# Kernel optimization log

Hardware: AMD Instinct MI355X
Metric: run time of the kernel (lower is better)

## Reference

```python
import jax, jax.numpy as jnp
import numpy as np
import math

B, S, HID = 2, 4096, 768
H, D, M = 12, 64, 64  # heads, head_dim, num_landmarks
CK = 33  # conv kernel size


def setup_inputs() -> dict:
    key = jax.random.key(0)
    ks = jax.random.split(key, 4)
    x = jax.random.normal(ks[0], (B, S, HID), dtype=jnp.float32)
    qkv_w = jax.random.normal(ks[1], (3 * HID, HID), dtype=jnp.float32) * 0.02
    qkv_b = jnp.zeros((3 * HID,), dtype=jnp.float32)
    conv_w = jax.random.normal(ks[2], (H, 1, CK, 1), dtype=jnp.float32) * 0.02
    out_w = jax.random.normal(ks[3], (HID, HID), dtype=jnp.float32) * 0.02
    out_b = jnp.zeros((HID,), dtype=jnp.float32)
    return {"x": x, "qkv_w": qkv_w, "qkv_b": qkv_b, "conv_w": conv_w,
            "out_w": out_w, "out_b": out_b}


def iterative_inv(mat, n_iter=6):
    # Newton-Schulz pseudo-inverse on [B,H,M,M]
    I = jnp.eye(mat.shape[-1], dtype=mat.dtype)
    K = mat
    a = jnp.abs(K)
    scale = 1.0 / (jnp.max(jnp.sum(a, axis=-2)) * jnp.max(jnp.sum(a, axis=-1)))
    V = scale * jnp.swapaxes(K, -1, -2)
    for _ in range(n_iter):
        KV = K @ V
        V = 0.25 * V @ (13.0 * I - KV @ (15.0 * I - KV @ (7.0 * I - KV)))
    return V


def reference(x, qkv_w, qkv_b, conv_w, out_w, out_b):
    scale = 1.0 / math.sqrt(D)
    qkv = x @ qkv_w.T + qkv_b  # [B,S,3*HID]
    q, k, v = jnp.split(qkv, 3, axis=-1)
    # [B,H,S,D]
    Q = q.reshape(B, S, H, D).transpose(0, 2, 1, 3)
    K = k.reshape(B, S, H, D).transpose(0, 2, 1, 3)
    V = v.reshape(B, S, H, D).transpose(0, 2, 1, 3)
    # landmark means over contiguous segments of size S//M
    seg = S // M
    Q_l = Q.reshape(B, H, M, seg, D).mean(axis=-2)  # [B,H,M,D]
    K_l = K.reshape(B, H, M, seg, D).mean(axis=-2)
    kernel_1 = jax.nn.softmax(jnp.einsum('bhsd,bhmd->bhsm', Q, K_l) * scale, axis=-1)
    kernel_2 = jax.nn.softmax(jnp.einsum('bhmd,bhnd->bhmn', Q_l, K_l) * scale, axis=-1)
    kernel_3 = jax.nn.softmax(jnp.einsum('bhmd,bhsd->bhms', Q_l, K) * scale, axis=-1)
    X = kernel_1 @ (iterative_inv(kernel_2) @ (kernel_3 @ V))  # [B,H,S,D]
    # depthwise conv over sequence dim: NCHW with C=H, spatial=(S,D), kernel (CK,1)
    pad = CK // 2
    conv_out = jax.lax.conv_general_dilated(
        V, conv_w, window_strides=(1, 1), padding=((pad, pad), (0, 0)),
        dimension_numbers=('NCHW', 'OIHW', 'NCHW'), feature_group_count=H)
    X = X + conv_out
    X = X.transpose(0, 2, 1, 3).reshape(B, S, HID)
    X = X @ out_w.T + out_b
    return X
```

## Files before the change

kernel.cpp:

```cpp
#include <hip/hip_runtime.h>
#include <math.h>

#define B_   2
#define S_   4096
#define HID_ 768
#define H_   12
#define D_   64
#define M_   64
#define CK_  33
#define BH_  (B_*H_)
#define KD_  768
#define NCH_ 32
#define SC_  128

typedef float  f32x4  __attribute__((ext_vector_type(4)));
typedef _Float16 f16x8 __attribute__((ext_vector_type(8)));
typedef unsigned short u16;

__device__ __forceinline__ u16 f2h_bits(float f) {
  union { _Float16 h; u16 u; } c; c.h = (_Float16)f; return c.u;
}
__device__ __forceinline__ float h2f(u16 b) {
  union { _Float16 h; u16 u; } c; c.u = b; return (float)c.h;
}
__device__ __forceinline__ void cvt8_hl(const float4 a, const float4 b,
                                        f16x8* hi, f16x8* lo) {
  const float v[8] = {a.x, a.y, a.z, a.w, b.x, b.y, b.z, b.w};
  f16x8 H, L;
#pragma unroll
  for (int e = 0; e < 8; ++e) {
    const _Float16 hh = (_Float16)v[e];
    H[e] = hh;
    L[e] = (_Float16)(v[e] - (float)hh);
  }
  *hi = H; *lo = L;
}

__device__ __forceinline__ void gld16(const void* g, void* l) {
  __builtin_amdgcn_global_load_lds(
      (const __attribute__((address_space(1))) void*)g,
      (__attribute__((address_space(3))) void*)l, 16, 0, 0);
}

#define N8X  786432
#define N8WQ 221184
#define N8WO 73728
__global__ __launch_bounds__(256) void split3(
    const float* __restrict__ x, const float* __restrict__ qkv_w,
    const float* __restrict__ out_w,
    u16* __restrict__ Xh, u16* __restrict__ Wqh, u16* __restrict__ Woh)
{
  const int i = blockIdx.x * 256 + threadIdx.x;
  const float* src; u16* dst; int j;
  if (i < N8X)                 { src = x;     dst = Xh;  j = i; }
  else if (i < N8X + N8WQ)     { src = qkv_w; dst = Wqh; j = i - N8X; }
  else if (i < N8X + N8WQ + N8WO) { src = out_w; dst = Woh; j = i - N8X - N8WQ; }
  else return;
  const float4 a = ((const float4*)src)[2 * j], b = ((const float4*)src)[2 * j + 1];
  const float v[8] = {a.x, a.y, a.z, a.w, b.x, b.y, b.z, b.w};
  union { u16 u[8]; uint4 q; } hv;
#pragma unroll
  for (int e = 0; e < 8; ++e) hv.u[e] = f2h_bits(v[e]);
  ((uint4*)dst)[j] = hv.q;
}

template<int MODE, int PROD>
__global__ __launch_bounds__(256) void gemm_mfma(
    const u16* __restrict__ Ahg, const u16* __restrict__ Alg,
    const u16* __restrict__ Bhg,
    const float* __restrict__ bias,
    float* __restrict__ oF, u16* __restrict__ oQ, u16* __restrict__ oK,
    u16* __restrict__ oV,
    float* __restrict__ Ql, float* __restrict__ Kl, u16* __restrict__ Klh)
{
  constexpr int BM = (MODE == 0) ? 128 : 64;
  constexpr int BN = (MODE == 0) ? 64 : 128;
  constexpr int NBX = (MODE == 0) ? 36 : 6;
  constexpr int WM = BM / 2, WN = BN / 2;
  constexpr int MF = WM / 16, NF = WN / 16;
  constexpr int AINST = BM / 64, BINST = BN / 64;
  constexpr int ABUF = BM * 32;
  constexpr int BUFSZ = ABUF * PROD + BN * 32;
  constexpr int NT = KD_ / 32;
  constexpr int NWG = NBX * (8192 / BM);
  constexpr int CPX = NWG / 8;
  constexpr int NLOADS = AINST * PROD + BINST;

  __shared__ __align__(16) u16 lds[2][BUFSZ];

  const int tid = threadIdx.x;
  const int lin = blockIdx.y * NBX + blockIdx.x;
  const int swb = (lin & 7) * CPX + (lin >> 3);
  const int m0 = (swb / NBX) * BM;
  const int n0 = (swb % NBX) * BN;

  const int wave = tid >> 6, lane = tid & 63;
  const int wm = wave >> 1, wn = wave & 1;
  const int lr = lane & 15, kg = lane >> 4;

  const int srow = tid >> 2;
  const int swz_s = (tid >> 3) & 3;
  const int sk = ((tid & 3) ^ swz_s) * 8;

  const u16* pAh = Ahg + (size_t)(m0 + srow) * KD_ + sk;
  const u16* pAl = (PROD == 2) ? (Alg + (size_t)(m0 + srow) * KD_ + sk) : nullptr;
  const u16* pBh = Bhg + (size_t)(n0 + srow) * KD_ + sk;

  f32x4 acc[MF][NF];
#pragma unroll
  for (int i = 0; i < MF; ++i)
#pragma unroll
    for (int j = 0; j < NF; ++j) acc[i][j] = (f32x4){0.f, 0.f, 0.f, 0.f};

  const int rsw = (lr >> 1) & 3;
  const int kq = (kg ^ rsw) * 8;
  const int abase = (wm * WM + lr) * 32 + kq;
  const int bbase = (wn * WN + lr) * 32 + kq;

#define STAGE_(buf, kt) do {                                              \
    const size_t go_ = (size_t)(kt) * 32;                                 \
    u16* L_ = &lds[buf][0];                                               \
    gld16(pAh + go_, L_ + tid * 8);                                       \
    if (AINST == 2) gld16(pAh + go_ + 64 * KD_, L_ + 2048 + tid * 8);     \
    if (PROD == 2) {                                                      \
      gld16(pAl + go_, L_ + ABUF + tid * 8);                              \
      if (AINST == 2) gld16(pAl + go_ + 64 * KD_, L_ + ABUF + 2048 + tid * 8); \
    }                                                                     \
    gld16(pBh + go_, L_ + ABUF * PROD + tid * 8);                         \
    if (BINST == 2) gld16(pBh + go_ + 64 * KD_, L_ + ABUF * PROD + 2048 + tid * 8); \
  } while (0)

  STAGE_(0, 0);

  int cur = 0;
  for (int kt = 0; kt < NT; ++kt) {
    if (kt + 1 < NT) {
      STAGE_(cur ^ 1, kt + 1);
      if constexpr (NLOADS == 3)
        asm volatile("s_waitcnt vmcnt(3)" ::: "memory");
      else
        asm volatile("s_waitcnt vmcnt(4)" ::: "memory");
    } else {
      asm volatile("s_waitcnt vmcnt(0)" ::: "memory");
    }
    __builtin_amdgcn_s_barrier();
    __builtin_amdgcn_sched_barrier(0);

    const u16* L_ = &lds[cur][0];
    f16x8 ah[MF], al[MF], bh[NF];
#pragma unroll
    for (int i = 0; i < MF; ++i) {
      ah[i] = *(const f16x8*)&L_[abase + i * 512];
      if (PROD == 2) al[i] = *(const f16x8*)&L_[ABUF + abase + i * 512];
    }
#pragma unroll
    for (int j = 0; j < NF; ++j)
      bh[j] = *(const f16x8*)&L_[ABUF * PROD + bbase + j * 512];
#pragma unroll
    for (int i = 0; i < MF; ++i)
#pragma unroll
      for (int j = 0; j < NF; ++j) {
        acc[i][j] = __builtin_amdgcn_mfma_f32_16x16x32_f16(ah[i], bh[j], acc[i][j], 0, 0, 0);
        if (PROD == 2)
          acc[i][j] = __builtin_amdgcn_mfma_f32_16x16x32_f16(al[i], bh[j], acc[i][j], 0, 0, 0);
      }

    __builtin_amdgcn_sched_barrier(0);
    __builtin_amdgcn_s_barrier();
    cur ^= 1;
  }
#undef STAGE_

  if (MODE == 0) {
    const int part = n0 / 768;
    const int h0 = (n0 - part * 768) >> 6;
    u16* base = (part == 0) ? oQ : ((part == 1) ? oK : oV);
#pragma unroll
    for (int i = 0; i < MF; ++i) {
      const int mbase = m0 + wm * WM + i * 16 + kg * 4;
#pragma unroll
      for (int j = 0; j < NF; ++j) {
        const int d = wn * WN + j * 16 + lr;
        const float bv = bias[n0 + d];
#pragma unroll
        for (int r = 0; r < 4; ++r) {
          const int row = mbase + r;
          const int b = row >> 12, s = row & (S_ - 1);
          base[(((size_t)(b * H_ + h0) * S_ + s) << 6) + d] = f2h_bits(acc[i][j][r] + bv);
        }
      }
    }
    if (part < 2) {
      const int rowseg = m0 + wm * WM;
      const int b = rowseg >> 12;
      const int seg = (rowseg & (S_ - 1)) >> 6;
      const int bhh = b * H_ + h0;
      float* dst = (part == 0) ? Ql : Kl;
#pragma unroll
      for (int j = 0; j < NF; ++j) {
        float sj = 0.f;
#pragma unroll
        for (int i = 0; i < MF; ++i)
#pragma unroll
          for (int r = 0; r < 4; ++r) sj += acc[i][j][r];
        sj += __shfl_xor(sj, 16);
        sj += __shfl_xor(sj, 32);
        if (kg == 0) {
          const int d = wn * WN + j * 16 + lr;
          const float lm = sj * (1.f / 64.f) + bias[n0 + d];
          dst[((size_t)bhh * M_ + seg) * 64 + d] = lm;
          if (part == 1) Klh[((size_t)bhh * M_ + seg) * 64 + d] = f2h_bits(lm);
        }
      }
    }
  } else {
#pragma unroll
    for (int i = 0; i < MF; ++i) {
      const int mbase = m0 + wm * WM + i * 16 + kg * 4;
#pragma unroll
      for (int j = 0; j < NF; ++j) {
        const int ncol = n0 + wn * WN + j * 16 + lr;
        const float bv = bias[ncol];
#pragma unroll
        for (int r = 0; r < 4; ++r) {
          const int row = mbase + r;
          oF[(size_t)row * HID_ + ncol] = acc[i][j][r] + bv;
        }
      }
    }
  }
}

__global__ __launch_bounds__(256) void kernel2_softmax(
    const float* __restrict__ Ql, const float* __restrict__ Kl,
    float* __restrict__ K2, float* __restrict__ colmax, float* __restrict__ rowmax)
{
  __shared__ float Qs[64][68], Ks[64][68], S2[64][68];
  __shared__ float red1[64], red2[64];
  const int bh = blockIdx.x, tid = threadIdx.x;
  for (int idx = tid; idx < 4096; idx += 256) {
    const int r = idx >> 6, c = idx & 63;
    Qs[r][c] = Ql[(size_t)bh * 4096 + idx];
    Ks[r][c] = Kl[(size_t)bh * 4096 + idx];
  }
  __syncthreads();
  for (int idx = tid; idx < 4096; idx += 256) {
    const int r = idx >> 6, c = idx & 63;
    float dot = 0.f;
#pragma unroll
    for (int k = 0; k < 64; k += 4) {
      const float4 a = *(const float4*)&Qs[r][k];
      const float4 b = *(const float4*)&Ks[c][k];
      dot += a.x * b.x + a.y * b.y + a.z * b.z + a.w * b.w;
    }
    S2[r][c] = dot * 0.125f;
  }
  __syncthreads();
  if (tid < 64) {
    const int r = tid;
    float mx = -1e30f;
    for (int c = 0; c < 64; ++c) mx = fmaxf(mx, S2[r][c]);
    float sum = 0.f;
    for (int c = 0; c < 64; ++c) { const float e = expf(S2[r][c] - mx); S2[r][c] = e; sum += e; }
    const float inv = 1.f / sum;
    for (int c = 0; c < 64; ++c) S2[r][c] *= inv;
  }
  __syncthreads();
  for (int idx = tid; idx < 4096; idx += 256)
    K2[(size_t)bh * 4096 + idx] = S2[idx >> 6][idx & 63];
  if (tid < 64) {
    float cs = 0.f, rs = 0.f;
    for (int m = 0; m < 64; ++m) { cs += S2[m][tid]; rs += S2[tid][m]; }
    red1[tid] = cs; red2[tid] = rs;
  }
  __syncthreads();
  if (tid == 0) {
    float mc = 0.f, mr = 0.f;
    for (int i = 0; i < 64; ++i) { mc = fmaxf(mc, red1[i]); mr = fmaxf(mr, red2[i]); }
    colmax[bh] = mc; rowmax[bh] = mr;
  }
}

__device__ inline void mm64w(float (*C)[68], float (*A)[68], float (*B)[68], int tid)
{
  const int r0 = (tid >> 4) * 2;
  const int c0 = (tid & 15) * 4;
  float acc[2][4];
#pragma unroll
  for (int i = 0; i < 2; ++i)
#pragma unroll
    for (int j = 0; j < 4; ++j) acc[i][j] = 0.f;
  for (int k = 0; k < 64; k += 4) {
    float4 a[2], b[4];
#pragma unroll
    for (int i = 0; i < 2; ++i) a[i] = *(const float4*)&A[r0 + i][k];
#pragma unroll
    for (int j = 0; j < 4; ++j) b[j] = *(const float4*)&B[k + j][c0];
    const float bb[4][4] = {{b[0].x, b[0].y, b[0].z, b[0].w},
                            {b[1].x, b[1].y, b[1].z, b[1].w},
                            {b[2].x, b[2].y, b[2].z, b[2].w},
                            {b[3].x, b[3].y, b[3].z, b[3].w}};
    const float aa[2][4] = {{a[0].x, a[0].y, a[0].z, a[0].w},
                            {a[1].x, a[1].y, a[1].z, a[1].w}};
#pragma unroll
    for (int i = 0; i < 2; ++i)
#pragma unroll
      for (int j = 0; j < 4; ++j)
#pragma unroll
        for (int kk = 0; kk < 4; ++kk) acc[i][j] += aa[i][kk] * bb[kk][j];
  }
#pragma unroll
  for (int i = 0; i < 2; ++i)
    *(float4*)&C[r0 + i][c0] = make_float4(acc[i][0], acc[i][1], acc[i][2], acc[i][3]);
}

__global__ __launch_bounds__(512) void newton_combine(
    const float* __restrict__ K2, const float* __restrict__ colmax,
    const float* __restrict__ rowmax,
    const float* __restrict__ Opart, const float* __restrict__ mpart,
    const float* __restrict__ lpart, float* __restrict__ W2)
{
  __shared__ float A_[64][68], V_[64][68], KV_[64][68], T_[64][68], U_[64][68];
  __shared__ float scale_s;
  const int bh = blockIdx.x, tid = threadIdx.x;
  if (tid == 0) {
    float mc = 0.f, mr = 0.f;
    for (int i = 0; i < BH_; ++i) { mc = fmaxf(mc, colmax[i]); mr = fmaxf(mr, rowmax[i]); }
    scale_s = 1.f / (mc * mr);
  }
  for (int idx = tid; idx < 4096; idx += 512)
    A_[idx >> 6][idx & 63] = K2[(size_t)bh * 4096 + idx];
  __syncthreads();
  const float scale = scale_s;
  for (int idx = tid; idx < 4096; idx += 512) {
    const int r = idx >> 6, c = idx & 63;
    V_[r][c] = scale * A_[c][r];
  }
  __syncthreads();
  for (int it = 0; it < 6; ++it) {
    mm64w(KV_, A_, V_, tid); __syncthreads();
    for (int idx = tid; idx < 4096; idx += 512) {
      const int r = idx >> 6, c = idx & 63;
      T_[r][c] = (r == c ? 7.f : 0.f) - KV_[r][c];
    }
    __syncthreads();
    mm64w(U_, KV_, T_, tid); __syncthreads();
    for (int idx = tid; idx < 4096; idx += 512) {
      const int r = idx >> 6, c = idx & 63;
      T_[r][c] = (r == c ? 15.f : 0.f) - U_[r][c];
    }
    __syncthreads();
    mm64w(U_, KV_, T_, tid); __syncthreads();
    for (int idx = tid; idx < 4096; idx += 512) {
      const int r = idx >> 6, c = idx & 63;
      T_[r][c] = (r == c ? 13.f : 0.f) - U_[r][c];
    }
    __syncthreads();
    mm64w(U_, V_, T_, tid); __syncthreads();
    for (int idx = tid; idx < 4096; idx += 512) {
      const int r = idx >> 6, c = idx & 63;
      V_[r][c] = 0.25f * U_[r][c];
    }
    __syncthreads();
  }
  float (*W1s)[68] = A_;
  float (*C_)[68]  = KV_;
  float (*w_)[68]  = T_;
  if (tid < 64) {
    const int m = tid;
    float M = -1e30f;
    for (int j = 0; j < NCH_; ++j)
      M = fmaxf(M, mpart[((size_t)bh * NCH_ + j) * 64 + m]);
    float denom = 0.f;
    for (int j = 0; j < NCH_; ++j)
      denom += expf(mpart[((size_t)bh * NCH_ + j) * 64 + m] - M) *
               lpart[((size_t)bh * NCH_ + j) * 64 + m];
    const float inv = 1.f / denom;
    for (int j = 0; j < NCH_; ++j)
      w_[m][j] = expf(mpart[((size_t)bh * NCH_ + j) * 64 + m] - M) * inv;
  }
  __syncthreads();
  const int mgB = tid >> 4, dq = (tid & 15) * 4;
#pragma unroll
  for (int i = 0; i < 2; ++i) {
    const int m = mgB + 32 * i;
    float4 acc = make_float4(0.f, 0.f, 0.f, 0.f);
    for (int j = 0; j < NCH_; ++j) {
      const float ww = w_[m][j];
      const float4 o = *(const float4*)&Opart[(((size_t)bh * NCH_ + j) * 64 + m) * 64 + dq];
      acc.x += ww * o.x; acc.y += ww * o.y; acc.z += ww * o.z; acc.w += ww * o.w;
    }
    *(float4*)&W1s[m][dq] = acc;
  }
  __syncthreads();
  mm64w(C_, V_, W1s, tid);
  __syncthreads();
  for (int idx = tid; idx < 4096; idx += 512)
    W2[(size_t)bh * 4096 + idx] = C_[idx >> 6][idx & 63];
}

__global__ __launch_bounds__(256) void k3v_pass1(
    const float* __restrict__ Ql, const u16* __restrict__ Kh,
    const u16* __restrict__ Vh, float* __restrict__ Opart,
    float* __restrict__ mpart, float* __restrict__ lpart)
{
  __shared__ float P[64][129];
  __shared__ float red1[64][4], red2[64][4];

  const int ch = blockIdx.x;
  const int bh = blockIdx.y;
  const int tid = threadIdx.x;
  const int wave = tid >> 6, lane = tid & 63;
  const int lr = lane & 15, kg = lane >> 4;

  const float* Qlb = Ql + (size_t)bh * 4096;
  const u16*   Kb  = Kh + (size_t)bh * S_ * 64;
  const u16*   Vb  = Vh + (size_t)bh * S_ * 64;

  f16x8 ah[4][2], al[4][2];
#pragma unroll
  for (int mt = 0; mt < 4; ++mt)
#pragma unroll
    for (int kk = 0; kk < 2; ++kk) {
      const float* qr = Qlb + (size_t)(mt * 16 + lr) * 64 + kk * 32 + kg * 8;
      cvt8_hl(*(const float4*)qr, *(const float4*)(qr + 4), &ah[mt][kk], &al[mt][kk]);
    }

#pragma unroll
  for (int t = 0; t < 2; ++t) {
    const int s0 = (wave * 2 + t) * 16;
    const int srow = ch * SC_ + s0 + lr;
    f32x4 acc[4];
#pragma unroll
    for (int mt = 0; mt < 4; ++mt) acc[mt] = (f32x4){0.f, 0.f, 0.f, 0.f};
#pragma unroll
    for (int kk = 0; kk < 2; ++kk) {
      const f16x8 bhf = *(const f16x8*)&Kb[(size_t)srow * 64 + kk * 32 + kg * 8];
#pragma unroll
      for (int mt = 0; mt < 4; ++mt) {
        acc[mt] = __builtin_amdgcn_mfma_f32_16x16x32_f16(ah[mt][kk], bhf, acc[mt], 0, 0, 0);
        acc[mt] = __builtin_amdgcn_mfma_f32_16x16x32_f16(al[mt][kk], bhf, acc[mt], 0, 0, 0);
      }
    }
#pragma unroll
    for (int mt = 0; mt < 4; ++mt)
#pragma unroll
      for (int r = 0; r < 4; ++r)
        P[mt * 16 + kg * 4 + r][s0 + lr] = acc[mt][r] * 0.125f;
  }
  __syncthreads();

  const int r = tid >> 2, q = tid & 3;
  {
    float mx = -1e30f;
#pragma unroll
    for (int s = 0; s < 32; ++s) mx = fmaxf(mx, P[r][q * 32 + s]);
    red1[r][q] = mx;
  }
  __syncthreads();
  const float rowmax = fmaxf(fmaxf(red1[r][0], red1[r][1]),
                             fmaxf(red1[r][2], red1[r][3]));
  {
    float sum = 0.f;
#pragma unroll
    for (int s = 0; s < 32; ++s) {
      const float e = expf(P[r][q * 32 + s] - rowmax);
      P[r][q * 32 + s] = e;
      sum += e;
    }
    red2[r][q] = sum;
  }
  __syncthreads();
  if (q == 0) {
    const float rowsum = red2[r][0] + red2[r][1] + red2[r][2] + red2[r][3];
    mpart[((size_t)bh * NCH_ + ch) * 64 + r] = rowmax;
    lpart[((size_t)bh * NCH_ + ch) * 64 + r] = rowsum;
  }

  const int mg = tid >> 4, dq = (tid & 15) * 4;
  float4 oacc[4];
#pragma unroll
  for (int i = 0; i < 4; ++i) oacc[i] = make_float4(0.f, 0.f, 0.f, 0.f);
  for (int s = 0; s < SC_; ++s) {
    const ushort4 vv = *(const ushort4*)&Vb[(size_t)(ch * SC_ + s) * 64 + dq];
    const float4 v = make_float4(h2f(vv.x), h2f(vv.y), h2f(vv.z), h2f(vv.w));
#pragma unroll
    for (int i = 0; i < 4; ++i) {
      const float p = P[mg * 4 + i][s];
      oacc[i].x += p * v.x; oacc[i].y += p * v.y;
      oacc[i].z += p * v.z; oacc[i].w += p * v.w;
    }
  }
#pragma unroll
  for (int i = 0; i < 4; ++i) {
    const size_t o = (((size_t)bh * NCH_ + ch) * 64 + mg * 4 + i) * 64 + dq;
    *(float4*)&Opart[o] = oacc[i];
  }
}

__global__ __launch_bounds__(256) void attn_conv_fused(
    const u16* __restrict__ Qh, const u16* __restrict__ Klh,
    const float* __restrict__ W2, const u16* __restrict__ Vh,
    const float* __restrict__ cw,
    u16* __restrict__ Xch, u16* __restrict__ Xcl)
{
  __shared__ __align__(16) u16 smem[19456];
  __shared__ float cws[33];

  const int ch = blockIdx.x;
  const int bh = blockIdx.y;
  const int tid = threadIdx.x;
  const int wave = tid >> 6, lane = tid & 63;
  const int lr = lane & 15, kg = lane >> 4;
  const int b = bh / H_, h = bh % H_;
  const int s0 = ch * 128;

  u16* Ph   = smem;
  u16* W2Th = smem + 9728;
  u16* W2Tl = smem + 14592;

  if (tid < 33) cws[tid] = cw[h * 33 + tid];
  for (int idx = tid; idx < 4096; idx += 256) {
    const int m = idx >> 6, d = idx & 63;
    const float w = W2[(size_t)bh * 4096 + idx];
    const _Float16 hh = (_Float16)w;
    W2Th[d * 76 + m] = f2h_bits(w);
    W2Tl[d * 76 + m] = f2h_bits(w - (float)hh);
  }

  const u16* Klb = Klh + (size_t)bh * 4096;
  const u16* Qb  = Qh + (size_t)bh * S_ * 64;
  f16x8 bf[4][2];
#pragma unroll
  for (int nt = 0; nt < 4; ++nt)
#pragma unroll
    for (int kk = 0; kk < 2; ++kk)
      bf[nt][kk] = *(const f16x8*)&Klb[(size_t)(nt * 16 + lr) * 64 + kk * 32 + kg * 8];

  f32x4 sacc[2][4];
#pragma unroll
  for (int t = 0; t < 2; ++t) {
#pragma unroll
    for (int nt = 0; nt < 4; ++nt) sacc[t][nt] = (f32x4){0.f, 0.f, 0.f, 0.f};
    const int rloc = wave * 32 + t * 16;
    f16x8 af[2];
#pragma unroll
    for (int kk = 0; kk < 2; ++kk)
      af[kk] = *(const f16x8*)&Qb[(size_t)(s0 + rloc + lr) * 64 + kk * 32 + kg * 8];
#pragma unroll
    for (int kk = 0; kk < 2; ++kk)
#pragma unroll
      for (int nt = 0; nt < 4; ++nt)
        sacc[t][nt] = __builtin_amdgcn_mfma_f32_16x16x32_f16(af[kk], bf[nt][kk], sacc[t][nt], 0, 0, 0);
  }

#pragma unroll
  for (int t = 0; t < 2; ++t)
#pragma unroll
    for (int nt = 0; nt < 4; ++nt)
      sacc[t][nt] *= 0.125f;

  float rinv[2][4];
#pragma unroll
  for (int t = 0; t < 2; ++t) {
#pragma unroll
    for (int r = 0; r < 4; ++r) {
      float mx = fmaxf(fmaxf(sacc[t][0][r], sacc[t][1][r]),
                       fmaxf(sacc[t][2][r], sacc[t][3][r]));
      mx = fmaxf(mx, __shfl_xor(mx, 1));
      mx = fmaxf(mx, __shfl_xor(mx, 2));
      mx = fmaxf(mx, __shfl_xor(mx, 4));
      mx = fmaxf(mx, __shfl_xor(mx, 8));
      float sum = 0.f;
#pragma unroll
      for (int nt = 0; nt < 4; ++nt) {
        const float e = expf(sacc[t][nt][r] - mx);
        sacc[t][nt][r] = e;
        sum += e;
      }
      sum += __shfl_xor(sum, 1);
      sum += __shfl_xor(sum, 2);
      sum += __shfl_xor(sum, 4);
      sum += __shfl_xor(sum, 8);
      rinv[t][r] = 1.f / sum;
    }
  }

#pragma unroll
  for (int t = 0; t < 2; ++t)
#pragma unroll
    for (int nt = 0; nt < 4; ++nt)
#pragma unroll
      for (int r = 0; r < 4; ++r) {
        const int row = wave * 32 + t * 16 + kg * 4 + r;
        Ph[row * 76 + nt * 16 + lr] = f2h_bits(sacc[t][nt][r] * rinv[t][r]);
      }
  __syncthreads();

  f32x4 oacc[2][4];
#pragma unroll
  for (int t = 0; t < 2; ++t)
#pragma unroll
    for (int dt = 0; dt < 4; ++dt) oacc[t][dt] = (f32x4){0.f, 0.f, 0.f, 0.f};
#pragma unroll
  for (int kk = 0; kk < 2; ++kk) {
    f16x8 pa[2];
#pragma unroll
    for (int t = 0; t < 2; ++t)
      pa[t] = *(const f16x8*)&Ph[(wave * 32 + t * 16 + lr) * 76 + kk * 32 + kg * 8];
#pragma unroll
    for (int dt = 0; dt < 4; ++dt) {
      const f16x8 wh = *(const f16x8*)&W2Th[(dt * 16 + lr) * 76 + kk * 32 + kg * 8];
      const f16x8 wl = *(const f16x8*)&W2Tl[(dt * 16 + lr) * 76 + kk * 32 + kg * 8];
#pragma unroll
      for (int t = 0; t < 2; ++t) {
        oacc[t][dt] = __builtin_amdgcn_mfma_f32_16x16x32_f16(pa[t], wh, oacc[t][dt], 0, 0, 0);
        oacc[t][dt] = __builtin_amdgcn_mfma_f32_16x16x32_f16(pa[t], wl, oacc[t][dt], 0, 0, 0);
      }
    }
  }
  __syncthreads();

  float* O = (float*)smem;
#pragma unroll
  for (int t = 0; t < 2; ++t)
#pragma unroll
    for (int dt = 0; dt < 4; ++dt)
#pragma unroll
      for (int r = 0; r < 4; ++r) {
        const int row = wave * 32 + t * 16 + kg * 4 + r;
        O[row * 68 + dt * 16 + lr] = oacc[t][dt][r];
      }
  __syncthreads();

  const int d = tid & 63, rg = tid >> 6;
  const int rbase = s0 + rg * 32;
  const u16* Vd = Vh + (size_t)bh * S_ * 64 + d;

  float v[40];
#pragma unroll
  for (int j = 0; j < 40; ++j) {
    const int sv = rbase - 16 + j;
    v[j] = (sv >= 0 && sv < S_) ? h2f(Vd[(size_t)sv * 64]) : 0.f;
  }

#pragma clang loop unroll(disable)
  for (int c = 0; c < 4; ++c) {
#pragma unroll
    for (int rr = 0; rr < 8; ++rr) {
      float acc = 0.f;
#pragma unroll
      for (int t = 0; t < 33; ++t) acc += v[rr + t] * cws[t];
      const int row = rg * 32 + c * 8 + rr;
      const float oo = O[row * 68 + d] + acc;
      const size_t idx = ((size_t)(b * S_ + s0 + row)) * HID_ + h * 64 + d;
      const u16 hh = f2h_bits(oo);
      Xch[idx] = hh;
      Xcl[idx] = f2h_bits(oo - h2f(hh));
    }
    if (c < 3) {
#pragma unroll
      for (int j = 0; j < 32; ++j) v[j] = v[j + 8];
#pragma unroll
      for (int j = 0; j < 8; ++j) {
        const int sv = rbase + 24 + c * 8 + j;
        v[32 + j] = (sv >= 0 && sv < S_) ? h2f(Vd[(size_t)sv * 64]) : 0.f;
      }
    }
  }
}

extern "C" void kernel_launch(void* const* d_in, const int* in_sizes, int n_in,
                              void* d_out, int out_size, void* d_ws, size_t ws_size,
                              hipStream_t stream)
{
  (void)in_sizes; (void)n_in; (void)out_size; (void)ws_size;
  const float* x      = (const float*)d_in[0];
  const float* qkv_w  = (const float*)d_in[1];
  const float* qkv_b  = (const float*)d_in[2];
  const float* conv_w = (const float*)d_in[3];
  const float* out_w  = (const float*)d_in[4];
  const float* out_b  = (const float*)d_in[5];
  float* out = (float*)d_out;

  float* ws = (float*)d_ws;
  u16* Qh = (u16*)ws;
  u16* Kh = Qh + 6291456;
  u16* Vh = Kh + 6291456;
  float* Ql = ws + 9437184;
  float* Kl = Ql + 98304;
  float* K2 = Kl + 98304;
  float* W2 = K2 + 98304;
  float* colmax = W2 + 98304;
  float* rowmax = colmax + 32;
  u16* Klh = (u16*)(rowmax + 32);
  float* nxt = rowmax + 32 + 49152;
  u16* Xh  = (u16*)nxt;
  u16* Xl  = Xh + 6291456;
  u16* Wqh = Xl + 6291456;
  u16* Woh = Wqh + 1769472;
  u16* Xch = Xh;
  u16* Xcl = Xl;
  float* Opart = (float*)Xh;
  float* mpart = (float*)Xl;
  float* lpart = mpart + BH_ * NCH_ * 64;

  split3<<<(N8X + N8WQ + N8WO + 255) / 256, 256, 0, stream>>>(
      x, qkv_w, out_w, Xh, Wqh, Woh);

  gemm_mfma<0, 1><<<dim3(36, 64), 256, 0, stream>>>(
      Xh, nullptr, Wqh, qkv_b, nullptr, Qh, Kh, Vh, Ql, Kl, Klh);

  kernel2_softmax<<<BH_, 256, 0, stream>>>(Ql, Kl, K2, colmax, rowmax);

  k3v_pass1<<<dim3(NCH_, BH_), 256, 0, stream>>>(Ql, Kh, Vh, Opart, mpart, lpart);

  newton_combine<<<BH_, 512, 0, stream>>>(K2, colmax, rowmax,
                                          Opart, mpart, lpart, W2);

  attn_conv_fused<<<dim3(NCH_, BH_), 256, 0, stream>>>(
      Qh, Klh, W2, Vh, conv_w, Xch, Xcl);

  gemm_mfma<1, 2><<<dim3(6, 128), 256, 0, stream>>>(
      Xch, Xcl, Woh, out_b, out, nullptr, nullptr, nullptr,
      nullptr, nullptr, nullptr);
}
```

Before: 238.9 us.

## Run Newton-Schulz inverse matmuls on MFMA with split-fp16 operands

```diff
diff --git a/kernel.cpp b/kernel.cpp
--- a/kernel.cpp
+++ b/kernel.cpp
@@ -34,6 +34,11 @@
     L[e] = (_Float16)(v[e] - (float)hh);
   }
   *hi = H; *lo = L;
+}
+__device__ __forceinline__ void wsplit(u16* Hh, u16* Hl, int idx, float v) {
+  const _Float16 hh = (_Float16)v;
+  Hh[idx] = f2h_bits(v);
+  Hl[idx] = f2h_bits(v - (float)hh);
 }
 
 __device__ __forceinline__ void gld16(const void* g, void* l) {
@@ -281,122 +286,154 @@
   }
 }
 
-__device__ inline void mm64w(float (*C)[68], float (*A)[68], float (*B)[68], int tid)
+#define NST 88
+__device__ __forceinline__ void mfma64x64(
+    const u16* Ah, const u16* Al, const u16* Bh, const u16* Bl,
+    int wave, int lr, int kg, f32x4 C[4])
 {
-  const int r0 = (tid >> 4) * 2;
-  const int c0 = (tid & 15) * 4;
-  float acc[2][4];
-#pragma unroll
-  for (int i = 0; i < 2; ++i)
-#pragma unroll
-    for (int j = 0; j < 4; ++j) acc[i][j] = 0.f;
-  for (int k = 0; k < 64; k += 4) {
-    float4 a[2], b[4];
-#pragma unroll
-    for (int i = 0; i < 2; ++i) a[i] = *(const float4*)&A[r0 + i][k];
-#pragma unroll
-    for (int j = 0; j < 4; ++j) b[j] = *(const float4*)&B[k + j][c0];
-    const float bb[4][4] = {{b[0].x, b[0].y, b[0].z, b[0].w},
-                            {b[1].x, b[1].y, b[1].z, b[1].w},
-                            {b[2].x, b[2].y, b[2].z, b[2].w},
-                            {b[3].x, b[3].y, b[3].z, b[3].w}};
-    const float aa[2][4] = {{a[0].x, a[0].y, a[0].z, a[0].w},
-                            {a[1].x, a[1].y, a[1].z, a[1].w}};
-#pragma unroll
-    for (int i = 0; i < 2; ++i)
-#pragma unroll
-      for (int j = 0; j < 4; ++j)
-#pragma unroll
-        for (int kk = 0; kk < 4; ++kk) acc[i][j] += aa[i][kk] * bb[kk][j];
-  }
-#pragma unroll
-  for (int i = 0; i < 2; ++i)
-    *(float4*)&C[r0 + i][c0] = make_float4(acc[i][0], acc[i][1], acc[i][2], acc[i][3]);
-}
-
-__global__ __launch_bounds__(512) void newton_combine(
+#pragma unroll
+  for (int j = 0; j < 4; ++j) C[j] = (f32x4){0.f, 0.f, 0.f, 0.f};
+#pragma unroll
+  for (int kk = 0; kk < 2; ++kk) {
+    const int ao = (wave * 16 + lr) * NST + kk * 32 + kg * 8;
+    const f16x8 ah = *(const f16x8*)&Ah[ao];
+    const f16x8 al = *(const f16x8*)&Al[ao];
+#pragma unroll
+    for (int j = 0; j < 4; ++j) {
+      const int bo = (j * 16 + lr) * NST + kk * 32 + kg * 8;
+      const f16x8 bh = *(const f16x8*)&Bh[bo];
+      const f16x8 bl = *(const f16x8*)&Bl[bo];
+      C[j] = __builtin_amdgcn_mfma_f32_16x16x32_f16(ah, bh, C[j], 0, 0, 0);
+      C[j] = __builtin_amdgcn_mfma_f32_16x16x32_f16(ah, bl, C[j], 0, 0, 0);
+      C[j] = __builtin_amdgcn_mfma_f32_16x16x32_f16(al, bh, C[j], 0, 0, 0);
+    }
+  }
+}
+
+__global__ __launch_bounds__(256) void newton_combine(
     const float* __restrict__ K2, const float* __restrict__ colmax,
     const float* __restrict__ rowmax,
     const float* __restrict__ Opart, const float* __restrict__ mpart,
     const float* __restrict__ lpart, float* __restrict__ W2)
 {
-  __shared__ float A_[64][68], V_[64][68], KV_[64][68], T_[64][68], U_[64][68];
+  __shared__ __align__(16) u16 K2h[64*NST], K2l[64*NST];
+  __shared__ __align__(16) u16 Vh_[64*NST], Vl_[64*NST];
+  __shared__ __align__(16) u16 VTh[64*NST], VTl[64*NST];
+  __shared__ __align__(16) u16 KVh[64*NST], KVl[64*NST];
+  __shared__ __align__(16) u16 TTh[64*NST], TTl[64*NST];
+  __shared__ float w_[64][33];
   __shared__ float scale_s;
+
   const int bh = blockIdx.x, tid = threadIdx.x;
+  const int wave = tid >> 6, lane = tid & 63;
+  const int lr = lane & 15, kg = lane >> 4;
+
   if (tid == 0) {
     float mc = 0.f, mr = 0.f;
     for (int i = 0; i < BH_; ++i) { mc = fmaxf(mc, colmax[i]); mr = fmaxf(mr, rowmax[i]); }
     scale_s = 1.f / (mc * mr);
   }
-  for (int idx = tid; idx < 4096; idx += 512)
-    A_[idx >> 6][idx & 63] = K2[(size_t)bh * 4096 + idx];
   __syncthreads();
   const float scale = scale_s;
-  for (int idx = tid; idx < 4096; idx += 512) {
+
+  for (int idx = tid; idx < 4096; idx += 256) {
     const int r = idx >> 6, c = idx & 63;
-    V_[r][c] = scale * A_[c][r];
-  }
-  __syncthreads();
+    const float v = K2[(size_t)bh * 4096 + idx];
+    wsplit(K2h, K2l, r * NST + c, v);
+    const float sv = scale * v;
+    wsplit(VTh, VTl, r * NST + c, sv);
+    wsplit(Vh_, Vl_, c * NST + r, sv);
+  }
+  __syncthreads();
+
+  f32x4 C[4];
   for (int it = 0; it < 6; ++it) {
-    mm64w(KV_, A_, V_, tid); __syncthreads();
-    for (int idx = tid; idx < 4096; idx += 512) {
-      const int r = idx >> 6, c = idx & 63;
-      T_[r][c] = (r == c ? 7.f : 0.f) - KV_[r][c];
-    }
+    mfma64x64(K2h, K2l, VTh, VTl, wave, lr, kg, C);
+#pragma unroll
+    for (int j = 0; j < 4; ++j)
+#pragma unroll
+      for (int r = 0; r < 4; ++r) {
+        const int row = wave * 16 + kg * 4 + r, col = j * 16 + lr;
+        const float kv = C[j][r];
+        wsplit(KVh, KVl, row * NST + col, kv);
+        wsplit(TTh, TTl, col * NST + row, (row == col ? 7.f : 0.f) - kv);
+      }
     __syncthreads();
-    mm64w(U_, KV_, T_, tid); __syncthreads();
-    for (int idx = tid; idx < 4096; idx += 512) {
-      const int r = idx >> 6, c = idx & 63;
-      T_[r][c] = (r == c ? 15.f : 0.f) - U_[r][c];
-    }
+    mfma64x64(KVh, KVl, TTh, TTl, wave, lr, kg, C);
     __syncthreads();
-    mm64w(U_, KV_, T_, tid); __syncthreads();
-    for (int idx = tid; idx < 4096; idx += 512) {
-      const int r = idx >> 6, c = idx & 63;
-      T_[r][c] = (r == c ? 13.f : 0.f) - U_[r][c];
-    }
+#pragma unroll
+    for (int j = 0; j < 4; ++j)
+#pragma unroll
+      for (int r = 0; r < 4; ++r) {
+        const int row = wave * 16 + kg * 4 + r, col = j * 16 + lr;
+        wsplit(TTh, TTl, col * NST + row, (row == col ? 15.f : 0.f) - C[j][r]);
+      }
     __syncthreads();
-    mm64w(U_, V_, T_, tid); __syncthreads();
-    for (int idx = tid; idx < 4096; idx += 512) {
-      const int r = idx >> 6, c = idx & 63;
-      V_[r][c] = 0.25f * U_[r][c];
-    }
+    mfma64x64(KVh, KVl, TTh, TTl, wave, lr, kg, C);
     __syncthreads();
-  }
-  float (*W1s)[68] = A_;
-  float (*C_)[68]  = KV_;
-  float (*w_)[68]  = T_;
+#pragma unroll
+    for (int j = 0; j < 4; ++j)
+#pragma unroll
+      for (int r = 0; r < 4; ++r) {
+        const int row = wave * 16 + kg * 4 + r, col = j * 16 + lr;
+        wsplit(TTh, TTl, col * NST + row, (row == col ? 13.f : 0.f) - C[j][r]);
+      }
+    __syncthreads();
+    mfma64x64(Vh_, Vl_, TTh, TTl, wave, lr, kg, C);
+#pragma unroll
+    for (int j = 0; j < 4; ++j)
+#pragma unroll
+      for (int r = 0; r < 4; ++r) {
+        const int row = wave * 16 + kg * 4 + r, col = j * 16 + lr;
+        const float v = 0.25f * C[j][r];
+        wsplit(Vh_, Vl_, row * NST + col, v);
+        wsplit(VTh, VTl, col * NST + row, v);
+      }
+    __syncthreads();
+  }
+
   if (tid < 64) {
     const int m = tid;
-    float M = -1e30f;
+    float Mx = -1e30f;
     for (int j = 0; j < NCH_; ++j)
-      M = fmaxf(M, mpart[((size_t)bh * NCH_ + j) * 64 + m]);
+      Mx = fmaxf(Mx, mpart[((size_t)bh * NCH_ + j) * 64 + m]);
     float denom = 0.f;
     for (int j = 0; j < NCH_; ++j)
-      denom += expf(mpart[((size_t)bh * NCH_ + j) * 64 + m] - M) *
+      denom += expf(mpart[((size_t)bh * NCH_ + j) * 64 + m] - Mx) *
                lpart[((size_t)bh * NCH_ + j) * 64 + m];
     const float inv = 1.f / denom;
     for (int j = 0; j < NCH_; ++j)
-      w_[m][j] = expf(mpart[((size_t)bh * NCH_ + j) * 64 + m] - M) * inv;
-  }
-  __syncthreads();
-  const int mgB = tid >> 4, dq = (tid & 15) * 4;
-#pragma unroll
-  for (int i = 0; i < 2; ++i) {
-    const int m = mgB + 32 * i;
-    float4 acc = make_float4(0.f, 0.f, 0.f, 0.f);
-    for (int j = 0; j < NCH_; ++j) {
-      const float ww = w_[m][j];
-      const float4 o = *(const float4*)&Opart[(((size_t)bh * NCH_ + j) * 64 + m) * 64 + dq];
-      acc.x += ww * o.x; acc.y += ww * o.y; acc.z += ww * o.z; acc.w += ww * o.w;
-    }
-    *(float4*)&W1s[m][dq] = acc;
-  }
-  __syncthreads();
-  mm64w(C_, V_, W1s, tid);
-  __syncthreads();
-  for (int idx = tid; idx < 4096; idx += 512)
-    W2[(size_t)bh * 4096 + idx] = C_[idx >> 6][idx & 63];
+      w_[m][j] = expf(mpart[((size_t)bh * NCH_ + j) * 64 + m] - Mx) * inv;
+  }
+  __syncthreads();
+  u16* W1Th = K2h;
+  u16* W1Tl = K2l;
+  {
+    const int mg = tid >> 4, dq = (tid & 15) * 4;
+#pragma unroll
+    for (int i = 0; i < 4; ++i) {
+      const int m = mg * 4 + i;
+      float4 acc = make_float4(0.f, 0.f, 0.f, 0.f);
+      for (int j = 0; j < NCH_; ++j) {
+        const float ww = w_[m][j];
+        const float4 o = *(const float4*)&Opart[(((size_t)bh * NCH_ + j) * 64 + m) * 64 + dq];
+        acc.x += ww * o.x; acc.y += ww * o.y; acc.z += ww * o.z; acc.w += ww * o.w;
+      }
+      wsplit(W1Th, W1Tl, (dq + 0) * NST + m, acc.x);
+      wsplit(W1Th, W1Tl, (dq + 1) * NST + m, acc.y);
+      wsplit(W1Th, W1Tl, (dq + 2) * NST + m, acc.z);
+      wsplit(W1Th, W1Tl, (dq + 3) * NST + m, acc.w);
+    }
+  }
+  __syncthreads();
+  mfma64x64(Vh_, Vl_, W1Th, W1Tl, wave, lr, kg, C);
+#pragma unroll
+  for (int j = 0; j < 4; ++j)
+#pragma unroll
+    for (int r = 0; r < 4; ++r) {
+      const int row = wave * 16 + kg * 4 + r, col = j * 16 + lr;
+      W2[(size_t)bh * 4096 + row * 64 + col] = C[j][r];
+    }
 }
 
 __global__ __launch_bounds__(256) void k3v_pass1(
@@ -715,7 +752,7 @@
 
   k3v_pass1<<<dim3(NCH_, BH_), 256, 0, stream>>>(Ql, Kh, Vh, Opart, mpart, lpart);
 
-  newton_combine<<<BH_, 512, 0, stream>>>(K2, colmax, rowmax,
+  newton_combine<<<BH_, 256, 0, stream>>>(K2, colmax, rowmax,
                                           Opart, mpart, lpart, W2);
 
   attn_conv_fused<<<dim3(NCH_, BH_), 256, 0, stream>>>(
```

Result: faster. 212.3 us (-11.1%).
